# Kernel tuning notes

Measured on AMD Instinct MI355X. Metric: run time of the kernel, lower is better.

Reference implementation:

```python
import jax, jax.numpy as jnp
import numpy as np

B, T, C = 16, 512, 32
W = 128            # max_window
SERIES_LEN = 100000
WIN_MIN, WIN_MAX = 2.0, 64.0
SHARP = 1.0        # fixed sharpness of the soft window edge
BN_EPS = 1e-5


def setup_inputs() -> dict:
    key = jax.random.key(0)
    ks = jax.random.split(key, 6)
    x = jax.random.normal(ks[0], (B, T, C), jnp.float32)
    full_series = jax.random.normal(ks[1], (SERIES_LEN, C), jnp.float32)
    # starts >= W so the lookback window never needs padding; end = start + T
    starts = jax.random.randint(ks[2], (B,), W, SERIES_LEN - T)
    indices = jnp.stack([starts, starts + T], axis=1).astype(jnp.int32)  # (B, 2)
    # raw (logit-space) per-channel window sizes, as in the torch init
    raw_win_mean = jax.random.normal(ks[3], (C,), jnp.float32)
    raw_win_std = jax.random.normal(ks[4], (C,), jnp.float32)
    return dict(
        x=x, full_series=full_series, indices=indices,
        raw_win_mean=raw_win_mean, raw_win_std=raw_win_std,
        gamma_mean=jnp.ones((C,), jnp.float32), beta_mean=jnp.zeros((C,), jnp.float32),
        gamma_std=jnp.ones((C,), jnp.float32), beta_std=jnp.zeros((C,), jnp.float32),
    )


def _soft_window_weights(raw_win):
    # sigmoid-mapped window size in [WIN_MIN, WIN_MAX], per channel
    win = WIN_MIN + jax.nn.sigmoid(raw_win) * (WIN_MAX - WIN_MIN)          # (C,)
    age = jnp.arange(W, dtype=jnp.float32)[::-1]                            # slot W-1 is most recent (age 0)
    w = jax.nn.sigmoid(SHARP * (win[None, :] - age[:, None]))               # (W, C)
    return w


def _rolling_windows(full_series, starts):
    # batch_windows[b] = full_series[starts[b]-W : starts[b]+T]   -> (B, W+T, C)
    offs = jnp.arange(W + T)
    bw = full_series[(starts - W)[:, None] + offs[None, :]]                 # (B, W+T, C)
    # window for output step t covers slots [t, t+W) (the W points before the current step)
    tidx = jnp.arange(T)[:, None] + jnp.arange(W)[None, :]                  # (T, W)
    return bw[:, tidx, :]                                                   # (B, T, W, C)


def _batchnorm(f, gamma, beta):
    # BatchNorm1d over (B, C, T): normalize per channel over batch and time, biased var
    mean = f.mean(axis=(0, 1))
    var = ((f - mean) ** 2).mean(axis=(0, 1))
    return (f - mean) * jax.lax.rsqrt(var + BN_EPS) * gamma + beta


def reference(x, full_series, indices, raw_win_mean, raw_win_std,
              gamma_mean, beta_mean, gamma_std, beta_std):
    starts = indices[:, 0]
    xw = _rolling_windows(full_series, starts)                              # (B, T, W, C)

    # feature 1: soft-window weighted mean
    w1 = _soft_window_weights(raw_win_mean)                                 # (W, C)
    s1 = jnp.sum(w1, axis=0)                                                # (C,)
    f_mean = jnp.einsum('btwc,wc->btc', xw, w1) / s1                        # (B, T, C)

    # feature 2: soft-window weighted std
    w2 = _soft_window_weights(raw_win_std)
    s2 = jnp.sum(w2, axis=0)
    m2 = jnp.einsum('btwc,wc->btc', xw, w2) / s2
    var2 = jnp.einsum('btwc,wc->btc', (xw - m2[:, :, None, :]) ** 2, w2) / s2
    f_std = jnp.sqrt(var2 + 1e-8)

    out_mean = _batchnorm(f_mean, gamma_mean, beta_mean)
    out_std = _batchnorm(f_std, gamma_std, beta_std)
    return jnp.concatenate([x, out_mean, out_std], axis=-1)                 # (B, T, 3*C)
```

## Files before the change

### kernel.cpp

```cpp
#include <hip/hip_runtime.h>
#include <math.h>

#define NB 16
#define NT 512
#define NC 32
#define NW 128
#define TILE_T 32
#define NTILES (NT / TILE_T)
#define NBLK (NB * NTILES)
#define NROWS (TILE_T + NW)
#define WIN_MIN_F 2.0f
#define WIN_RANGE_F 62.0f
#define EINV_F 0.36787944117f

#define WS_FMEAN 0
#define WS_FSTD  (NB*NT*NC)
#define WS_PART  (2*NB*NT*NC)

__device__ __forceinline__ float fast_sigmoid_neg(float a) {
    return __builtin_amdgcn_rcpf(1.0f + __expf(a));
}

__global__ __launch_bounds__(256) void feat_main(
    const float* __restrict__ series,
    const int*   __restrict__ indices,
    const float* __restrict__ rwm,
    const float* __restrict__ rws,
    float* __restrict__ f_mean,
    float* __restrict__ f_std,
    float* __restrict__ partials)
{
    __shared__ __align__(16) float s_x [NROWS * NC];
    __shared__ float s_w1[NW * NC];
    __shared__ float s_w2[NW * NC];
    __shared__ float s_win[2 * NC];
    __shared__ float s_red[4 * 8 * NC];

    const int tid = threadIdx.x;
    const int blk = blockIdx.x;
    const int b   = blk >> 4;
    const int tt  = blk & 15;
    const int t0  = tt * TILE_T;
    const int start = indices[2 * b];

    if (tid < 2 * NC) {
        const float raw = (tid < NC) ? rwm[tid] : rws[tid - NC];
        s_win[tid] = WIN_MIN_F + WIN_RANGE_F * fast_sigmoid_neg(-raw);
    }

    const float4* src4 = (const float4*)(series + (size_t)(start - NW + t0) * NC);
    float4* dst4 = (float4*)s_x;
#pragma unroll
    for (int k = 0; k < 5; ++k) {
        const int j = tid + k * 256;
        dst4[j] = src4[j];
    }
    __syncthreads();

    {
        const int c  = tid & 31;
        const int wc = tid >> 5;
        const int w0 = wc * 16;
        const float age0 = (float)(NW - 1 - w0);
        float E1 = __expf(age0 - s_win[c]);
        float E2 = __expf(age0 - s_win[NC + c]);
#pragma unroll
        for (int j = 0; j < 16; ++j) {
            const int idx = (w0 + j) * NC + c;
            s_w1[idx] = __builtin_amdgcn_rcpf(1.0f + E1);
            s_w2[idx] = __builtin_amdgcn_rcpf(1.0f + E2);
            E1 *= EINV_F;
            E2 *= EINV_F;
        }
    }
    __syncthreads();

    const int c  = tid & 31;
    const int tg = tid >> 5;
    const int tbase = tg * 4;

    float a1[4], a2[4], a3[4], xs[4], xq[4];
#pragma unroll
    for (int k = 0; k < 4; ++k) {
        a1[k] = 0.f; a2[k] = 0.f; a3[k] = 0.f;
        xs[k] = s_x[(tbase + k) * NC + c];
        xq[k] = xs[k] * xs[k];
    }

    float s1 = 0.f, s2 = 0.f;
#pragma unroll 8
    for (int w = 0; w < NW; ++w) {
        const float w1 = s_w1[w * NC + c];
        const float w2 = s_w2[w * NC + c];
        s1 += w1; s2 += w2;
#pragma unroll
        for (int k = 0; k < 4; ++k) {
            a1[k] = fmaf(xs[k], w1, a1[k]);
            a2[k] = fmaf(xs[k], w2, a2[k]);
            a3[k] = fmaf(xq[k], w2, a3[k]);
        }
        xs[0] = xs[1]; xs[1] = xs[2]; xs[2] = xs[3];
        xq[0] = xq[1]; xq[1] = xq[2]; xq[2] = xq[3];
        const float xn = s_x[(tbase + 4 + w) * NC + c];
        xs[3] = xn; xq[3] = xn * xn;
    }

    const float inv1 = __builtin_amdgcn_rcpf(s1);
    const float inv2 = __builtin_amdgcn_rcpf(s2);

    float p0 = 0.f, p1 = 0.f, p2 = 0.f, p3 = 0.f;
#pragma unroll
    for (int k = 0; k < 4; ++k) {
        const float fm = a1[k] * inv1;
        const float m2 = a2[k] * inv2;
        float var = a3[k] * inv2 - m2 * m2;
        var = fmaxf(var, 0.0f);
        const float fs = sqrtf(var + 1e-8f);
        const int t = t0 + tbase + k;
        const size_t o = ((size_t)b * NT + t) * NC + c;
        f_mean[o] = fm;
        f_std[o]  = fs;
        p0 += fm; p1 += fm * fm; p2 += fs; p3 += fs * fs;
    }

    s_red[(0 * 8 + tg) * NC + c] = p0;
    s_red[(1 * 8 + tg) * NC + c] = p1;
    s_red[(2 * 8 + tg) * NC + c] = p2;
    s_red[(3 * 8 + tg) * NC + c] = p3;
    __syncthreads();

    if (tid < 4 * NC) {
        const int a = tid >> 5, cc = tid & 31;
        float s = 0.f;
#pragma unroll
        for (int g = 0; g < 8; ++g) s += s_red[(a * 8 + g) * NC + cc];
        partials[blk * (4 * NC) + a * NC + cc] = s;
    }
}

__global__ __launch_bounds__(256) void bn_write(
    const float* __restrict__ x,
    const float* __restrict__ f_mean,
    const float* __restrict__ f_std,
    const float* __restrict__ partials,
    const float* __restrict__ gm, const float* __restrict__ bm,
    const float* __restrict__ gs, const float* __restrict__ bs,
    float* __restrict__ out)
{
    __shared__ __align__(16) float s_part[8 * 128];
    __shared__ __align__(16) float s_sums[128];
    __shared__ __align__(16) float s_coef[4 * NC];

    const int tid = threadIdx.x;

    {
        const int cell  = tid & 31;
        const int slice = tid >> 5;
        const float4* p4 = (const float4*)partials;
        float4 acc = {0.f, 0.f, 0.f, 0.f};
#pragma unroll 8
        for (int i = 0; i < 32; ++i) {
            const float4 v = p4[(slice * 32 + i) * 32 + cell];
            acc.x += v.x; acc.y += v.y; acc.z += v.z; acc.w += v.w;
        }
        *(float4*)&s_part[(slice * 32 + cell) * 4] = acc;
    }
    __syncthreads();
    if (tid < 32) {
        float4 s = {0.f, 0.f, 0.f, 0.f};
#pragma unroll
        for (int sl = 0; sl < 8; ++sl) {
            const float4 v = ((const float4*)s_part)[sl * 32 + tid];
            s.x += v.x; s.y += v.y; s.z += v.z; s.w += v.w;
        }
        ((float4*)s_sums)[tid] = s;
    }
    __syncthreads();
    if (tid < NC) {
        const float invN = 1.0f / (float)(NB * NT);
        const float mu_m  = s_sums[tid] * invN;
        float var_m = s_sums[32 + tid] * invN - mu_m * mu_m;
        var_m = fmaxf(var_m, 0.0f);
        const float A1 = gm[tid] / sqrtf(var_m + 1e-5f);
        const float B1 = bm[tid] - mu_m * A1;
        const float mu_s  = s_sums[64 + tid] * invN;
        float var_s = s_sums[96 + tid] * invN - mu_s * mu_s;
        var_s = fmaxf(var_s, 0.0f);
        const float A2 = gs[tid] / sqrtf(var_s + 1e-5f);
        const float B2 = bs[tid] - mu_s * A2;
        s_coef[tid]          = A1;
        s_coef[NC + tid]     = B1;
        s_coef[2 * NC + tid] = A2;
        s_coef[3 * NC + tid] = B2;
    }
    __syncthreads();

    const float4* x4  = (const float4*)x;
    const float4* fm4 = (const float4*)f_mean;
    const float4* fs4 = (const float4*)f_std;
    const float4* cf4 = (const float4*)s_coef;
    float4* out4 = (float4*)out;
    const int base = blockIdx.x * 768;

#pragma unroll
    for (int k = 0; k < 3; ++k) {
        const int j = base + tid + k * 256;
        const int row = j / 24;
        const int q = j - row * 24;
        float4 v;
        if (q < 8) {
            v = x4[row * 8 + q];
        } else if (q < 16) {
            const int m = q - 8;
            const float4 f = fm4[row * 8 + m];
            const float4 A = cf4[m], Bv = cf4[8 + m];
            v.x = fmaf(f.x, A.x, Bv.x); v.y = fmaf(f.y, A.y, Bv.y);
            v.z = fmaf(f.z, A.z, Bv.z); v.w = fmaf(f.w, A.w, Bv.w);
        } else {
            const int m = q - 16;
            const float4 f = fs4[row * 8 + m];
            const float4 A = cf4[16 + m], Bv = cf4[24 + m];
            v.x = fmaf(f.x, A.x, Bv.x); v.y = fmaf(f.y, A.y, Bv.y);
            v.z = fmaf(f.z, A.z, Bv.z); v.w = fmaf(f.w, A.w, Bv.w);
        }
        out4[j] = v;
    }
}

extern "C" void kernel_launch(void* const* d_in, const int* in_sizes, int n_in,
                              void* d_out, int out_size, void* d_ws, size_t ws_size,
                              hipStream_t stream) {
    const float* x      = (const float*)d_in[0];
    const float* series = (const float*)d_in[1];
    const int*   idx    = (const int*)d_in[2];
    const float* rwm    = (const float*)d_in[3];
    const float* rws    = (const float*)d_in[4];
    const float* gm     = (const float*)d_in[5];
    const float* bm     = (const float*)d_in[6];
    const float* gs     = (const float*)d_in[7];
    const float* bs     = (const float*)d_in[8];
    float* out = (float*)d_out;
    float* ws  = (float*)d_ws;

    float* f_mean   = ws + WS_FMEAN;
    float* f_std    = ws + WS_FSTD;
    float* partials = ws + WS_PART;

    feat_main<<<NBLK, 256, 0, stream>>>(series, idx, rwm, rws, f_mean, f_std, partials);
    bn_write<<<NBLK, 256, 0, stream>>>(x, f_mean, f_std, partials, gm, bm, gs, bs, out);
}
```

Baseline: 18.33 us.

## Use packed FP32 FMAs in window loop and move x copy into feature kernel

The inner sliding-window loop now has each thread handle two channels with packed v2f FMAs over two time rows, instead of one channel over four rows. This is meant to double FMA throughput per instruction via packed FP32 math. The passthrough copy of x into the output moves from the second kernel into the first, so it overlaps with the compute-bound stage and the second kernel shrinks. The reduction layout changes to 16 thread groups. The trade-off is less register-level reuse of x across rows, since each weight load is now shared by two rows rather than four.

```diff
diff --git a/kernel.cpp b/kernel.cpp
--- a/kernel.cpp
+++ b/kernel.cpp
@@ -17,24 +17,31 @@
 #define WS_FSTD  (NB*NT*NC)
 #define WS_PART  (2*NB*NT*NC)
 
+typedef float v2f __attribute__((ext_vector_type(2)));
+
 __device__ __forceinline__ float fast_sigmoid_neg(float a) {
     return __builtin_amdgcn_rcpf(1.0f + __expf(a));
 }
+__device__ __forceinline__ v2f pk_fma(v2f a, v2f b, v2f c) {
+    return __builtin_elementwise_fma(a, b, c);
+}
 
 __global__ __launch_bounds__(256) void feat_main(
+    const float* __restrict__ x,
     const float* __restrict__ series,
     const int*   __restrict__ indices,
     const float* __restrict__ rwm,
     const float* __restrict__ rws,
     float* __restrict__ f_mean,
     float* __restrict__ f_std,
-    float* __restrict__ partials)
+    float* __restrict__ partials,
+    float* __restrict__ out)
 {
     __shared__ __align__(16) float s_x [NROWS * NC];
-    __shared__ float s_w1[NW * NC];
-    __shared__ float s_w2[NW * NC];
+    __shared__ __align__(16) float s_w1[NW * NC];
+    __shared__ __align__(16) float s_w2[NW * NC];
     __shared__ float s_win[2 * NC];
-    __shared__ float s_red[4 * 8 * NC];
+    __shared__ __align__(16) float s_red[4 * 16 * NC];
 
     const int tid = threadIdx.x;
     const int blk = blockIdx.x;
@@ -42,6 +49,12 @@
     const int tt  = blk & 15;
     const int t0  = tt * TILE_T;
     const int start = indices[2 * b];
+
+    {
+        const int row = b * NT + t0 + (tid >> 3);
+        const int q = tid & 7;
+        ((float4*)out)[row * 24 + q] = ((const float4*)x)[row * 8 + q];
+    }
 
     if (tid < 2 * NC) {
         const float raw = (tid < NC) ? rwm[tid] : rws[tid - NC];
@@ -75,71 +88,84 @@
     }
     __syncthreads();
 
-    const int c  = tid & 31;
-    const int tg = tid >> 5;
-    const int tbase = tg * 4;
-
-    float a1[4], a2[4], a3[4], xs[4], xq[4];
-#pragma unroll
-    for (int k = 0; k < 4; ++k) {
-        a1[k] = 0.f; a2[k] = 0.f; a3[k] = 0.f;
-        xs[k] = s_x[(tbase + k) * NC + c];
-        xq[k] = xs[k] * xs[k];
-    }
-
-    float s1 = 0.f, s2 = 0.f;
-#pragma unroll 8
+    const int cp = tid & 15;
+    const int tg = tid >> 4;
+    const int r0 = tg * 2;
+
+    const v2f* xv  = (const v2f*)s_x;
+    const v2f* w1v = (const v2f*)s_w1;
+    const v2f* w2v = (const v2f*)s_w2;
+
+    v2f a1_0 = {0.f,0.f}, a2_0 = {0.f,0.f}, a3_0 = {0.f,0.f};
+    v2f a1_1 = {0.f,0.f}, a2_1 = {0.f,0.f}, a3_1 = {0.f,0.f};
+    v2f sw1 = {0.f,0.f}, sw2 = {0.f,0.f};
+
+    v2f x0 = xv[(r0 + 0) * 16 + cp];
+    v2f x1 = xv[(r0 + 1) * 16 + cp];
+    v2f q0 = x0 * x0;
+    v2f q1 = x1 * x1;
+
+#pragma unroll 4
     for (int w = 0; w < NW; ++w) {
-        const float w1 = s_w1[w * NC + c];
-        const float w2 = s_w2[w * NC + c];
-        s1 += w1; s2 += w2;
-#pragma unroll
-        for (int k = 0; k < 4; ++k) {
-            a1[k] = fmaf(xs[k], w1, a1[k]);
-            a2[k] = fmaf(xs[k], w2, a2[k]);
-            a3[k] = fmaf(xq[k], w2, a3[k]);
-        }
-        xs[0] = xs[1]; xs[1] = xs[2]; xs[2] = xs[3];
-        xq[0] = xq[1]; xq[1] = xq[2]; xq[2] = xq[3];
-        const float xn = s_x[(tbase + 4 + w) * NC + c];
-        xs[3] = xn; xq[3] = xn * xn;
-    }
-
-    const float inv1 = __builtin_amdgcn_rcpf(s1);
-    const float inv2 = __builtin_amdgcn_rcpf(s2);
-
-    float p0 = 0.f, p1 = 0.f, p2 = 0.f, p3 = 0.f;
-#pragma unroll
-    for (int k = 0; k < 4; ++k) {
-        const float fm = a1[k] * inv1;
-        const float m2 = a2[k] * inv2;
-        float var = a3[k] * inv2 - m2 * m2;
-        var = fmaxf(var, 0.0f);
-        const float fs = sqrtf(var + 1e-8f);
-        const int t = t0 + tbase + k;
-        const size_t o = ((size_t)b * NT + t) * NC + c;
-        f_mean[o] = fm;
-        f_std[o]  = fs;
-        p0 += fm; p1 += fm * fm; p2 += fs; p3 += fs * fs;
-    }
-
-    s_red[(0 * 8 + tg) * NC + c] = p0;
-    s_red[(1 * 8 + tg) * NC + c] = p1;
-    s_red[(2 * 8 + tg) * NC + c] = p2;
-    s_red[(3 * 8 + tg) * NC + c] = p3;
-    __syncthreads();
-
-    if (tid < 4 * NC) {
-        const int a = tid >> 5, cc = tid & 31;
-        float s = 0.f;
-#pragma unroll
-        for (int g = 0; g < 8; ++g) s += s_red[(a * 8 + g) * NC + cc];
-        partials[blk * (4 * NC) + a * NC + cc] = s;
+        const v2f wv1 = w1v[w * 16 + cp];
+        const v2f wv2 = w2v[w * 16 + cp];
+        sw1 = sw1 + wv1;
+        sw2 = sw2 + wv2;
+        a1_0 = pk_fma(x0, wv1, a1_0);
+        a2_0 = pk_fma(x0, wv2, a2_0);
+        a3_0 = pk_fma(q0, wv2, a3_0);
+        a1_1 = pk_fma(x1, wv1, a1_1);
+        a2_1 = pk_fma(x1, wv2, a2_1);
+        a3_1 = pk_fma(q1, wv2, a3_1);
+        const v2f xn = xv[(r0 + 2 + w) * 16 + cp];
+        x0 = x1; q0 = q1;
+        x1 = xn; q1 = xn * xn;
+    }
+
+    v2f inv1, inv2;
+    inv1.x = __builtin_amdgcn_rcpf(sw1.x); inv1.y = __builtin_amdgcn_rcpf(sw1.y);
+    inv2.x = __builtin_amdgcn_rcpf(sw2.x); inv2.y = __builtin_amdgcn_rcpf(sw2.y);
+
+    v2f p0 = {0.f,0.f}, p1 = {0.f,0.f}, p2 = {0.f,0.f}, p3 = {0.f,0.f};
+#pragma unroll
+    for (int k = 0; k < 2; ++k) {
+        const v2f A1 = k ? a1_1 : a1_0;
+        const v2f A2 = k ? a2_1 : a2_0;
+        const v2f A3 = k ? a3_1 : a3_0;
+        const v2f fm = A1 * inv1;
+        const v2f m2 = A2 * inv2;
+        const v2f e2 = A3 * inv2;
+        v2f fs;
+        fs.x = sqrtf(fmaxf(e2.x - m2.x * m2.x, 0.f) + 1e-8f);
+        fs.y = sqrtf(fmaxf(e2.y - m2.y * m2.y, 0.f) + 1e-8f);
+        const int row = t0 + r0 + k;
+        const size_t o2 = ((size_t)b * NT + row) * 16 + cp;
+        ((v2f*)f_mean)[o2] = fm;
+        ((v2f*)f_std)[o2]  = fs;
+        p0 = p0 + fm;
+        p1 = pk_fma(fm, fm, p1);
+        p2 = p2 + fs;
+        p3 = pk_fma(fs, fs, p3);
+    }
+
+    v2f* redv = (v2f*)s_red;
+    redv[(0 * 16 + tg) * 16 + cp] = p0;
+    redv[(1 * 16 + tg) * 16 + cp] = p1;
+    redv[(2 * 16 + tg) * 16 + cp] = p2;
+    redv[(3 * 16 + tg) * 16 + cp] = p3;
+    __syncthreads();
+
+    if (tid < 64) {
+        const int stat = tid >> 4, cc = tid & 15;
+        v2f s = {0.f, 0.f};
+#pragma unroll
+        for (int g = 0; g < 16; ++g)
+            s = s + redv[(stat * 16 + g) * 16 + cc];
+        ((v2f*)partials)[blk * 64 + stat * 16 + cc] = s;
     }
 }
 
 __global__ __launch_bounds__(256) void bn_write(
-    const float* __restrict__ x,
     const float* __restrict__ f_mean,
     const float* __restrict__ f_std,
     const float* __restrict__ partials,
@@ -195,35 +221,35 @@
     }
     __syncthreads();
 
-    const float4* x4  = (const float4*)x;
     const float4* fm4 = (const float4*)f_mean;
     const float4* fs4 = (const float4*)f_std;
     const float4* cf4 = (const float4*)s_coef;
     float4* out4 = (float4*)out;
-    const int base = blockIdx.x * 768;
-
-#pragma unroll
-    for (int k = 0; k < 3; ++k) {
-        const int j = base + tid + k * 256;
-        const int row = j / 24;
-        const int q = j - row * 24;
+    const int row0 = blockIdx.x * 32;
+
+#pragma unroll
+    for (int k = 0; k < 2; ++k) {
+        const int j = tid + k * 256;
+        const int r = j >> 4;
+        const int q = j & 15;
+        const int row = row0 + r;
         float4 v;
+        int oq;
         if (q < 8) {
-            v = x4[row * 8 + q];
-        } else if (q < 16) {
-            const int m = q - 8;
-            const float4 f = fm4[row * 8 + m];
-            const float4 A = cf4[m], Bv = cf4[8 + m];
+            const float4 f = fm4[row * 8 + q];
+            const float4 A = cf4[q], Bv = cf4[8 + q];
             v.x = fmaf(f.x, A.x, Bv.x); v.y = fmaf(f.y, A.y, Bv.y);
             v.z = fmaf(f.z, A.z, Bv.z); v.w = fmaf(f.w, A.w, Bv.w);
+            oq = 8 + q;
         } else {
-            const int m = q - 16;
+            const int m = q - 8;
             const float4 f = fs4[row * 8 + m];
             const float4 A = cf4[16 + m], Bv = cf4[24 + m];
             v.x = fmaf(f.x, A.x, Bv.x); v.y = fmaf(f.y, A.y, Bv.y);
             v.z = fmaf(f.z, A.z, Bv.z); v.w = fmaf(f.w, A.w, Bv.w);
-        }
-        out4[j] = v;
+            oq = 16 + m;
+        }
+        out4[row * 24 + oq] = v;
     }
 }
 
@@ -246,6 +272,6 @@
     float* f_std    = ws + WS_FSTD;
     float* partials = ws + WS_PART;
 
-    feat_main<<<NBLK, 256, 0, stream>>>(series, idx, rwm, rws, f_mean, f_std, partials);
-    bn_write<<<NBLK, 256, 0, stream>>>(x, f_mean, f_std, partials, gm, bm, gs, bs, out);
-}
+    feat_main<<<NBLK, 256, 0, stream>>>(x, series, idx, rwm, rws, f_mean, f_std, partials, out);
+    bn_write<<<NBLK, 256, 0, stream>>>(f_mean, f_std, partials, gm, bm, gs, bs, out);
+}
```

After: 17.29 us. -5.7%, faster.

## Replace saturated window weights with prefix sums and shorten weighted loop to 25 taps

Applied to the files above, without the earlier changes.

Sigmoid window weights whose value is effectively one are treated as exactly one. Their contribution comes from per-channel prefix sums of x and x^2 built in shared memory, so the explicit weighted loop covers only a 25-slot transition band starting at a per-channel offset. This replaces the 128-tap loop and the full weight tables. The x-copy part of the output is moved from the second kernel into the first. The change approximates weights below about 115-win as zero and above the band as one, which adds small numerical error.

```diff
diff --git a/kernel.cpp b/kernel.cpp
--- a/kernel.cpp
+++ b/kernel.cpp
@@ -9,32 +9,38 @@
 #define NTILES (NT / TILE_T)
 #define NBLK (NB * NTILES)
 #define NROWS (TILE_T + NW)
+#define PADROWS 169
+#define NTR 25
 #define WIN_MIN_F 2.0f
 #define WIN_RANGE_F 62.0f
-#define EINV_F 0.36787944117f
 
 #define WS_FMEAN 0
 #define WS_FSTD  (NB*NT*NC)
 #define WS_PART  (2*NB*NT*NC)
 
+typedef float v2f __attribute__((ext_vector_type(2)));
+
 __device__ __forceinline__ float fast_sigmoid_neg(float a) {
     return __builtin_amdgcn_rcpf(1.0f + __expf(a));
 }
 
 __global__ __launch_bounds__(256) void feat_main(
+    const float* __restrict__ x,
     const float* __restrict__ series,
     const int*   __restrict__ indices,
     const float* __restrict__ rwm,
     const float* __restrict__ rws,
     float* __restrict__ f_mean,
     float* __restrict__ f_std,
-    float* __restrict__ partials)
+    float* __restrict__ partials,
+    float* __restrict__ out)
 {
-    __shared__ __align__(16) float s_x [NROWS * NC];
-    __shared__ float s_w1[NW * NC];
-    __shared__ float s_w2[NW * NC];
+    __shared__ __align__(16) float s_x[PADROWS * NC];
+    __shared__ __align__(16) v2f   s_P[NROWS * NC];
+    __shared__ __align__(16) v2f   s_wt[NTR * NC];
     __shared__ float s_win[2 * NC];
-    __shared__ float s_red[4 * 8 * NC];
+    __shared__ int   s_wsi[2 * NC];
+    __shared__ float s_red[1024];
 
     const int tid = threadIdx.x;
     const int blk = blockIdx.x;
@@ -43,9 +49,18 @@
     const int t0  = tt * TILE_T;
     const int start = indices[2 * b];
 
+    {
+        const int row = b * NT + t0 + (tid >> 3);
+        const int q = tid & 7;
+        ((float4*)out)[row * 24 + q] = ((const float4*)x)[row * 8 + q];
+    }
+
     if (tid < 2 * NC) {
-        const float raw = (tid < NC) ? rwm[tid] : rws[tid - NC];
-        s_win[tid] = WIN_MIN_F + WIN_RANGE_F * fast_sigmoid_neg(-raw);
+        const int c = tid & 31;
+        const float raw = (tid < NC) ? rwm[c] : rws[c];
+        const float win = WIN_MIN_F + WIN_RANGE_F * fast_sigmoid_neg(-raw);
+        s_win[tid] = win;
+        s_wsi[tid] = (int)(115.0f - win);
     }
 
     const float4* src4 = (const float4*)(series + (size_t)(start - NW + t0) * NC);
@@ -55,91 +70,150 @@
         const int j = tid + k * 256;
         dst4[j] = src4[j];
     }
-    __syncthreads();
-
+    if (tid < 72) {
+        dst4[1280 + tid] = make_float4(0.f, 0.f, 0.f, 0.f);
+    }
+    __syncthreads();
+
+    const int c_s  = tid & 31;
+    const int seg  = tid >> 5;
+    float l1[20], l2[20];
     {
-        const int c  = tid & 31;
-        const int wc = tid >> 5;
-        const int w0 = wc * 16;
-        const float age0 = (float)(NW - 1 - w0);
-        float E1 = __expf(age0 - s_win[c]);
-        float E2 = __expf(age0 - s_win[NC + c]);
-#pragma unroll
-        for (int j = 0; j < 16; ++j) {
-            const int idx = (w0 + j) * NC + c;
-            s_w1[idx] = __builtin_amdgcn_rcpf(1.0f + E1);
-            s_w2[idx] = __builtin_amdgcn_rcpf(1.0f + E2);
-            E1 *= EINV_F;
-            E2 *= EINV_F;
+        float r1 = 0.f, r2 = 0.f;
+        const int base = (seg * 20) * NC + c_s;
+#pragma unroll
+        for (int i = 0; i < 20; ++i) {
+            l1[i] = r1; l2[i] = r2;
+            const float xv = s_x[base + i * NC];
+            r1 += xv;
+            r2 = fmaf(xv, xv, r2);
+        }
+        s_red[0 * 256 + seg * NC + c_s] = r1;
+        s_red[1 * 256 + seg * NC + c_s] = r2;
+    }
+
+    for (int i = tid; i < 2 * NTR * NC; i += 256) {
+        const int c = i & 31;
+        const int r = i >> 5;
+        const int tbl = (r >= NTR) ? 1 : 0;
+        const int j = r - NTR * tbl;
+        const int ws = s_wsi[tbl * NC + c];
+        const int w = ws + j;
+        float val = 0.f;
+        if (w < NW) {
+            const float age = (float)(NW - 1 - w);
+            val = fast_sigmoid_neg(age - s_win[tbl * NC + c]);
+        }
+        ((float*)s_wt)[(j * NC + c) * 2 + tbl] = val;
+    }
+    __syncthreads();
+
+    if (tid < 64) {
+        const int tbl = tid >> 5, c = tid & 31;
+        float o = 0.f;
+#pragma unroll
+        for (int s = 0; s < 8; ++s) {
+            const int idx = tbl * 256 + s * NC + c;
+            const float t = s_red[idx];
+            s_red[idx] = o;
+            o += t;
+        }
+    }
+    __syncthreads();
+
+    {
+        const float o1 = s_red[0 * 256 + seg * NC + c_s];
+        const float o2 = s_red[1 * 256 + seg * NC + c_s];
+#pragma unroll
+        for (int i = 0; i < 20; ++i) {
+            v2f p; p.x = o1 + l1[i]; p.y = o2 + l2[i];
+            s_P[(seg * 20 + i) * NC + c_s] = p;
         }
     }
     __syncthreads();
 
     const int c  = tid & 31;
-    const int tg = tid >> 5;
-    const int tbase = tg * 4;
-
-    float a1[4], a2[4], a3[4], xs[4], xq[4];
+    const int rg = tid >> 5;
+    const int r0 = rg * 4;
+    const int wsm = s_wsi[c];
+    const int wss = s_wsi[NC + c];
+
+    float a1[4] = {0.f,0.f,0.f,0.f};
+    float a2[4] = {0.f,0.f,0.f,0.f};
+    float a3[4] = {0.f,0.f,0.f,0.f};
+    float sw1 = 0.f, sw2 = 0.f;
+
+    const int bm_ = (r0 + wsm) * NC + c;
+    const int bs_ = (r0 + wss) * NC + c;
+    float xm[4], xv[4], qv[4];
 #pragma unroll
     for (int k = 0; k < 4; ++k) {
-        a1[k] = 0.f; a2[k] = 0.f; a3[k] = 0.f;
-        xs[k] = s_x[(tbase + k) * NC + c];
-        xq[k] = xs[k] * xs[k];
-    }
-
-    float s1 = 0.f, s2 = 0.f;
-#pragma unroll 8
-    for (int w = 0; w < NW; ++w) {
-        const float w1 = s_w1[w * NC + c];
-        const float w2 = s_w2[w * NC + c];
-        s1 += w1; s2 += w2;
+        xm[k] = s_x[bm_ + k * NC];
+        const float v = s_x[bs_ + k * NC];
+        xv[k] = v; qv[k] = v * v;
+    }
+
+#pragma unroll 5
+    for (int j = 0; j < NTR; ++j) {
+        const v2f wv = s_wt[j * NC + c];
+        sw1 += wv.x; sw2 += wv.y;
 #pragma unroll
         for (int k = 0; k < 4; ++k) {
-            a1[k] = fmaf(xs[k], w1, a1[k]);
-            a2[k] = fmaf(xs[k], w2, a2[k]);
-            a3[k] = fmaf(xq[k], w2, a3[k]);
-        }
-        xs[0] = xs[1]; xs[1] = xs[2]; xs[2] = xs[3];
-        xq[0] = xq[1]; xq[1] = xq[2]; xq[2] = xq[3];
-        const float xn = s_x[(tbase + 4 + w) * NC + c];
-        xs[3] = xn; xq[3] = xn * xn;
-    }
-
+            a1[k] = fmaf(xm[k], wv.x, a1[k]);
+            a2[k] = fmaf(xv[k], wv.y, a2[k]);
+            a3[k] = fmaf(qv[k], wv.y, a3[k]);
+        }
+        xm[0] = xm[1]; xm[1] = xm[2]; xm[2] = xm[3];
+        xm[3] = s_x[bm_ + (4 + j) * NC];
+        xv[0] = xv[1]; xv[1] = xv[2]; xv[2] = xv[3];
+        qv[0] = qv[1]; qv[1] = qv[2]; qv[2] = qv[3];
+        const float nv = s_x[bs_ + (4 + j) * NC];
+        xv[3] = nv; qv[3] = nv * nv;
+    }
+
+    const int wsm25 = (wsm + NTR < NW) ? wsm + NTR : NW;
+    const int wss25 = (wss + NTR < NW) ? wss + NTR : NW;
+    const float s1 = sw1 + (float)(NW - wsm25);
+    const float s2 = sw2 + (float)(NW - wss25);
     const float inv1 = __builtin_amdgcn_rcpf(s1);
     const float inv2 = __builtin_amdgcn_rcpf(s2);
 
     float p0 = 0.f, p1 = 0.f, p2 = 0.f, p3 = 0.f;
 #pragma unroll
     for (int k = 0; k < 4; ++k) {
-        const float fm = a1[k] * inv1;
-        const float m2 = a2[k] * inv2;
-        float var = a3[k] * inv2 - m2 * m2;
-        var = fmaxf(var, 0.0f);
+        const int t = r0 + k;
+        const v2f pe = s_P[(t + NW) * NC + c];
+        const v2f pm = s_P[(t + wsm25) * NC + c];
+        const v2f ps = s_P[(t + wss25) * NC + c];
+        const float A1 = a1[k] + (pe.x - pm.x);
+        const float A2 = a2[k] + (pe.x - ps.x);
+        const float A3 = a3[k] + (pe.y - ps.y);
+        const float fm = A1 * inv1;
+        const float m2 = A2 * inv2;
+        const float var = fmaxf(A3 * inv2 - m2 * m2, 0.f);
         const float fs = sqrtf(var + 1e-8f);
-        const int t = t0 + tbase + k;
-        const size_t o = ((size_t)b * NT + t) * NC + c;
+        const size_t o = ((size_t)(b * NT + t0 + t)) * NC + c;
         f_mean[o] = fm;
         f_std[o]  = fs;
-        p0 += fm; p1 += fm * fm; p2 += fs; p3 += fs * fs;
-    }
-
-    s_red[(0 * 8 + tg) * NC + c] = p0;
-    s_red[(1 * 8 + tg) * NC + c] = p1;
-    s_red[(2 * 8 + tg) * NC + c] = p2;
-    s_red[(3 * 8 + tg) * NC + c] = p3;
-    __syncthreads();
-
-    if (tid < 4 * NC) {
-        const int a = tid >> 5, cc = tid & 31;
+        p0 += fm; p1 = fmaf(fm, fm, p1); p2 += fs; p3 = fmaf(fs, fs, p3);
+    }
+
+    s_red[0 * 256 + rg * NC + c] = p0;
+    s_red[1 * 256 + rg * NC + c] = p1;
+    s_red[2 * 256 + rg * NC + c] = p2;
+    s_red[3 * 256 + rg * NC + c] = p3;
+    __syncthreads();
+
+    if (tid < 128) {
+        const int stat = tid >> 5, cc = tid & 31;
         float s = 0.f;
 #pragma unroll
-        for (int g = 0; g < 8; ++g) s += s_red[(a * 8 + g) * NC + cc];
-        partials[blk * (4 * NC) + a * NC + cc] = s;
+        for (int g = 0; g < 8; ++g) s += s_red[stat * 256 + g * NC + cc];
+        partials[blk * (4 * NC) + stat * NC + cc] = s;
     }
 }
 
 __global__ __launch_bounds__(256) void bn_write(
-    const float* __restrict__ x,
     const float* __restrict__ f_mean,
     const float* __restrict__ f_std,
     const float* __restrict__ partials,
@@ -195,35 +269,35 @@
     }
     __syncthreads();
 
-    const float4* x4  = (const float4*)x;
     const float4* fm4 = (const float4*)f_mean;
     const float4* fs4 = (const float4*)f_std;
     const float4* cf4 = (const float4*)s_coef;
     float4* out4 = (float4*)out;
-    const int base = blockIdx.x * 768;
-
-#pragma unroll
-    for (int k = 0; k < 3; ++k) {
-        const int j = base + tid + k * 256;
-        const int row = j / 24;
-        const int q = j - row * 24;
+    const int row0 = blockIdx.x * 32;
+
+#pragma unroll
+    for (int k = 0; k < 2; ++k) {
+        const int j = tid + k * 256;
+        const int r = j >> 4;
+        const int q = j & 15;
+        const int row = row0 + r;
         float4 v;
+        int oq;
         if (q < 8) {
-            v = x4[row * 8 + q];
-        } else if (q < 16) {
-            const int m = q - 8;
-            const float4 f = fm4[row * 8 + m];
-            const float4 A = cf4[m], Bv = cf4[8 + m];
+            const float4 f = fm4[row * 8 + q];
+            const float4 A = cf4[q], Bv = cf4[8 + q];
             v.x = fmaf(f.x, A.x, Bv.x); v.y = fmaf(f.y, A.y, Bv.y);
             v.z = fmaf(f.z, A.z, Bv.z); v.w = fmaf(f.w, A.w, Bv.w);
+            oq = 8 + q;
         } else {
-            const int m = q - 16;
+            const int m = q - 8;
             const float4 f = fs4[row * 8 + m];
             const float4 A = cf4[16 + m], Bv = cf4[24 + m];
             v.x = fmaf(f.x, A.x, Bv.x); v.y = fmaf(f.y, A.y, Bv.y);
             v.z = fmaf(f.z, A.z, Bv.z); v.w = fmaf(f.w, A.w, Bv.w);
-        }
-        out4[j] = v;
+            oq = 16 + m;
+        }
+        out4[row * 24 + oq] = v;
     }
 }
 
@@ -246,6 +320,6 @@
     float* f_std    = ws + WS_FSTD;
     float* partials = ws + WS_PART;
 
-    feat_main<<<NBLK, 256, 0, stream>>>(series, idx, rwm, rws, f_mean, f_std, partials);
-    bn_write<<<NBLK, 256, 0, stream>>>(x, f_mean, f_std, partials, gm, bm, gs, bs, out);
+    feat_main<<<NBLK, 256, 0, stream>>>(x, series, idx, rwm, rws, f_mean, f_std, partials, out);
+    bn_write<<<NBLK, 256, 0, stream>>>(f_mean, f_std, partials, gm, bm, gs, bs, out);
 }
```

Measured after the change: 15.08 us (median of 2 runs). 17.8% less time.
